# Kernel tuning notes

Hardware: AMD Instinct MI355X
Metric: run time of the kernel (lower is better)

Reference implementation:

```python
import math
import jax, jax.numpy as jnp
import numpy as np

B, QL, CL, D, H = 4, 2048, 2048, 512, 8  # batch, q_len, c_len, hidden/query/context dim, heads
A = D // H
SCALE = 1.0 / math.sqrt(D)
FILL = -100000.0


def setup_inputs() -> dict:
    key = jax.random.key(0)
    ks = jax.random.split(key, 6)
    query = jax.random.normal(ks[0], (B, QL, D), dtype=jnp.float32)
    context = jax.random.normal(ks[1], (B, CL, D), dtype=jnp.float32)
    mask = jax.random.randint(ks[2], (B, CL, H), 0, 2).astype(bool)
    Wq = (jax.random.normal(ks[3], (D, D)) * 0.02).astype(jnp.float32)    # Q: query_dim -> hidden_dim (no bias)
    Wkv = (jax.random.normal(ks[4], (D, 2 * D)) * 0.02).astype(jnp.float32)  # KV: context_dim -> 2*hidden_dim
    Wout = (jax.random.normal(ks[5], (D, D)) * 0.02).astype(jnp.float32)  # out: hidden_dim -> context_dim
    return {"query": query, "context": context, "mask": mask, "Wq": Wq, "Wkv": Wkv, "Wout": Wout}


def reference(query, context, mask, Wq, Wkv, Wout):
    b, q_len, _ = query.shape
    c_len = context.shape[1]
    q = (query @ Wq).reshape(b, q_len, H, A)
    kv = context @ Wkv
    k = kv[..., :D].reshape(b, c_len, H, A)
    v = kv[..., D:].reshape(b, c_len, H, A)
    # [b, q, k, h] scores
    scores = jnp.einsum('bqha,bkha->bqkh', q, k)
    # mask.unsqueeze(1): [b, 1, c_len, h]; apply_mask == where(mask, FILL, x)
    scores = jnp.where(mask[:, None, :, :], FILL, scores)
    attn_weights = jax.nn.softmax(scores * SCALE, axis=2)
    # NOTE: faithful to original torch einsum 'bqkh,bvha->bqha' (k and v are
    # independent summed indices, as in the source code).
    attn = jnp.einsum('bqkh,bvha->bqha', attn_weights, v)
    attn = attn.reshape(b, q_len, D)
    return attn @ Wout
```

## Files before the change

### kernel.cpp

```cpp
#include <hip/hip_runtime.h>

#define BATCH 4
#define QLEN 2048
#define CLEN 2048
#define DIM 512
#define NBLK1 512
#define CPB 128
#define RPC 16
#define NSL 8


__global__ __launch_bounds__(256) void k1_partial(const float* __restrict__ ctx,
                                                  float4* __restrict__ partial) {
    __shared__ float4 red[256];
    const int blk = blockIdx.x, t = threadIdx.x;
    const int b = blk >> 7, ch = blk & 127;
    const int rg = t >> 7, f4 = t & 127;
    const float4* src = reinterpret_cast<const float4*>(ctx)
                      + (size_t)(b * CLEN + ch * RPC) * (DIM / 4);
    float4 s = make_float4(0.f, 0.f, 0.f, 0.f);
#pragma unroll
    for (int i = 0; i < 8; ++i) {
        float4 x = src[(size_t)(rg + 2 * i) * (DIM / 4) + f4];
        s.x += x.x; s.y += x.y; s.z += x.z; s.w += x.w;
    }
    red[t] = s;
    __syncthreads();
    if (t < 128) {
        float4 a = red[t], c = red[t + 128];
        partial[(size_t)blk * (DIM / 4) + t] =
            make_float4(a.x + c.x, a.y + c.y, a.z + c.z, a.w + c.w);
    }
}

__global__ __launch_bounds__(256) void k2_middle(const float4* __restrict__ partial,
                                                 const float* __restrict__ Wkv,
                                                 const float* __restrict__ Wout,
                                                 float* __restrict__ opart) {
    __shared__ float4 red[256];
    __shared__ float cs[DIM];
    __shared__ float vl[256];
    __shared__ float vslice[64];
    const int blk = blockIdx.x, t = threadIdx.x;
    const int b1 = blk >> 3, sl = blk & 7;

    {
        const int g = t & 127, h = t >> 7;
        const float4* p = partial + (size_t)(b1 * CPB + h * 64) * (DIM / 4) + g;
        float4 s = make_float4(0.f, 0.f, 0.f, 0.f);
#pragma unroll 16
        for (int j = 0; j < 64; ++j) {
            float4 x = p[(size_t)j * (DIM / 4)];
            s.x += x.x; s.y += x.y; s.z += x.z; s.w += x.w;
        }
        red[t] = s;
    }
    __syncthreads();
    if (t < 128) {
        float4 a = red[t], c = red[t + 128];
        reinterpret_cast<float4*>(cs)[t] =
            make_float4(a.x + c.x, a.y + c.y, a.z + c.z, a.w + c.w);
    }
    __syncthreads();

    {
        const int el = t & 63, dg = t >> 6;
        const float* w = Wkv + (size_t)(dg * 128) * (2 * DIM) + DIM + sl * 64 + el;
        float s = 0.f;
#pragma unroll 8
        for (int d0 = 0; d0 < 128; ++d0)
            s += cs[dg * 128 + d0] * w[(size_t)d0 * (2 * DIM)];
        vl[t] = s;
    }
    __syncthreads();
    if (t < 64) vslice[t] = vl[t] + vl[t + 64] + vl[t + 128] + vl[t + 192];
    __syncthreads();

    {
#pragma unroll
        for (int half = 0; half < 2; ++half) {
            const int f = half * 256 + t;
            const float* w = Wout + (size_t)(sl * 64) * DIM + f;
            float s = 0.f;
#pragma unroll 8
            for (int e0 = 0; e0 < 64; ++e0)
                s += vslice[e0] * w[(size_t)e0 * DIM];
            opart[(size_t)(sl * BATCH + b1) * DIM + f] = s;
        }
    }
}

__global__ __launch_bounds__(256) void k3_bcast(const float4* __restrict__ opart4,
                                                float4* __restrict__ out) {
    const int blk = blockIdx.x, t = threadIdx.x;
    const int b = blk >> 8, qg = blk & 255;
    const int rg = t >> 7, f4 = t & 127;
    float4 v = make_float4(0.f, 0.f, 0.f, 0.f);
#pragma unroll
    for (int sl = 0; sl < NSL; ++sl) {
        float4 x = opart4[(size_t)(sl * BATCH + b) * (DIM / 4) + f4];
        v.x += x.x; v.y += x.y; v.z += x.z; v.w += x.w;
    }
    float4* dst = out + (size_t)(b * QLEN + qg * 8) * (DIM / 4);
#pragma unroll
    for (int i = 0; i < 4; ++i)
        dst[(size_t)(rg + 2 * i) * (DIM / 4) + f4] = v;
}

extern "C" void kernel_launch(void* const* d_in, const int* in_sizes, int n_in,
                              void* d_out, int out_size, void* d_ws, size_t ws_size,
                              hipStream_t stream) {
    const float* ctx  = (const float*)d_in[1];
    const float* Wkv  = (const float*)d_in[4];
    const float* Wout = (const float*)d_in[5];
    float* ws = (float*)d_ws;
    float* partial = ws;
    float* opart   = partial + (size_t)NBLK1 * DIM;

    k1_partial<<<NBLK1, 256, 0, stream>>>(ctx, (float4*)partial);
    k2_middle<<<BATCH * NSL, 256, 0, stream>>>((const float4*)partial, Wkv, Wout, opart);
    k3_bcast<<<BATCH * 256, 256, 0, stream>>>((const float4*)opart, (float4*)d_out);
}
```

Measured before the change: 26.75 us.

## Precompute Wv·Wout in parallel with context column sums; fuse finish into broadcast

The value half of Wkv is now premultiplied with Wout into a combined 512x512 matrix. That product runs in extra blocks of the same launch as the context column-sum stripes, so it overlaps with the memory-bound reduction. The middle and broadcast kernels merge into one 1024-block kernel: each block recomputes a 32-column slice of the output vector from the summed context and the combined weight, then writes its rows directly. This removes one launch and the serial 32-block middle stage. In exchange it does a full 512x512x512 weight GEMM on every call and repeats the small GEMV work in every finishing block.

New measurement: 35.04 us. +31.0%, slower.

```diff
diff --git a/kernel.cpp b/kernel.cpp
--- a/kernel.cpp
+++ b/kernel.cpp
@@ -4,107 +4,118 @@
 #define QLEN 2048
 #define CLEN 2048
 #define DIM 512
-#define NBLK1 512
-#define CPB 128
-#define RPC 16
-#define NSL 8
+#define NSTRIPE 512
+#define NGEMM 256
+#define NRC 8
 
 
-__global__ __launch_bounds__(256) void k1_partial(const float* __restrict__ ctx,
-                                                  float4* __restrict__ partial) {
-    __shared__ float4 red[256];
+__global__ __launch_bounds__(256) void k1_stripe_gemm(
+    const float* __restrict__ ctx, const float* __restrict__ Wkv,
+    const float* __restrict__ Wout, float4* __restrict__ partial4,
+    float* __restrict__ Wcomb)
+{
     const int blk = blockIdx.x, t = threadIdx.x;
-    const int b = blk >> 7, ch = blk & 127;
-    const int rg = t >> 7, f4 = t & 127;
-    const float4* src = reinterpret_cast<const float4*>(ctx)
-                      + (size_t)(b * CLEN + ch * RPC) * (DIM / 4);
-    float4 s = make_float4(0.f, 0.f, 0.f, 0.f);
+    if (blk < NSTRIPE) {
+        __shared__ float4 red[256];
+        const int b = blk >> 7, rc = (blk >> 4) & 7, cc = blk & 15;
+        const int r0 = t >> 3, c = t & 7;
+        const size_t rowbase = (size_t)(b * CLEN + rc * 256 + r0) * (DIM / 4);
+        const int f4 = cc * 8 + c;
+        float4 s = make_float4(0.f, 0.f, 0.f, 0.f);
 #pragma unroll
-    for (int i = 0; i < 8; ++i) {
-        float4 x = src[(size_t)(rg + 2 * i) * (DIM / 4) + f4];
-        s.x += x.x; s.y += x.y; s.z += x.z; s.w += x.w;
-    }
-    red[t] = s;
-    __syncthreads();
-    if (t < 128) {
-        float4 a = red[t], c = red[t + 128];
-        partial[(size_t)blk * (DIM / 4) + t] =
-            make_float4(a.x + c.x, a.y + c.y, a.z + c.z, a.w + c.w);
+        for (int i = 0; i < 8; ++i) {
+            float4 x = reinterpret_cast<const float4*>(ctx)
+                           [rowbase + (size_t)(32 * i) * (DIM / 4) + f4];
+            s.x += x.x; s.y += x.y; s.z += x.z; s.w += x.w;
+        }
+        red[t] = s;
+        __syncthreads();
+#pragma unroll
+        for (int st = 128; st >= 8; st >>= 1) {
+            if (t < st) {
+                float4 a = red[t], c4 = red[t + st];
+                red[t] = make_float4(a.x + c4.x, a.y + c4.y, a.z + c4.z, a.w + c4.w);
+            }
+            __syncthreads();
+        }
+        if (t < 8)
+            partial4[(size_t)(b * NRC + rc) * (DIM / 4) + cc * 8 + t] = red[t];
+    } else {
+        __shared__ float As[32 * 64];
+        __shared__ float Bs[64 * 32];
+        const int m = blk - NSTRIPE;
+        const int ti = m >> 4, tj = m & 15;
+        const int j = t & 31, i0 = (t >> 5) * 4;
+        float a0 = 0.f, a1 = 0.f, a2 = 0.f, a3 = 0.f;
+        for (int e0 = 0; e0 < DIM; e0 += 64) {
+#pragma unroll
+            for (int it = 0; it < 8; ++it) {
+                const int idx = it * 256 + t;
+                As[idx] = Wkv[(size_t)(ti * 32 + (idx >> 6)) * (2 * DIM) + DIM + e0 + (idx & 63)];
+                Bs[idx] = Wout[(size_t)(e0 + (idx >> 5)) * DIM + tj * 32 + (idx & 31)];
+            }
+            __syncthreads();
+#pragma unroll 16
+            for (int e = 0; e < 64; ++e) {
+                const float bv = Bs[e * 32 + j];
+                a0 += As[(i0 + 0) * 64 + e] * bv;
+                a1 += As[(i0 + 1) * 64 + e] * bv;
+                a2 += As[(i0 + 2) * 64 + e] * bv;
+                a3 += As[(i0 + 3) * 64 + e] * bv;
+            }
+            __syncthreads();
+        }
+        float* dst = Wcomb + (size_t)(ti * 32 + i0) * DIM + tj * 32 + j;
+        dst[0 * DIM] = a0; dst[1 * DIM] = a1; dst[2 * DIM] = a2; dst[3 * DIM] = a3;
     }
 }
 
-__global__ __launch_bounds__(256) void k2_middle(const float4* __restrict__ partial,
-                                                 const float* __restrict__ Wkv,
-                                                 const float* __restrict__ Wout,
-                                                 float* __restrict__ opart) {
-    __shared__ float4 red[256];
+__global__ __launch_bounds__(256) void k2_finish(
+    const float* __restrict__ partial, const float* __restrict__ Wcomb,
+    float4* __restrict__ out)
+{
     __shared__ float cs[DIM];
-    __shared__ float vl[256];
-    __shared__ float vslice[64];
+    __shared__ float rr[256];
+    __shared__ float os[32];
     const int blk = blockIdx.x, t = threadIdx.x;
-    const int b1 = blk >> 3, sl = blk & 7;
+    const int b = blk >> 8, fs = (blk >> 4) & 15, qc = blk & 15;
 
     {
-        const int g = t & 127, h = t >> 7;
-        const float4* p = partial + (size_t)(b1 * CPB + h * 64) * (DIM / 4) + g;
-        float4 s = make_float4(0.f, 0.f, 0.f, 0.f);
-#pragma unroll 16
-        for (int j = 0; j < 64; ++j) {
-            float4 x = p[(size_t)j * (DIM / 4)];
-            s.x += x.x; s.y += x.y; s.z += x.z; s.w += x.w;
+        float s0 = 0.f, s1 = 0.f;
+#pragma unroll
+        for (int rc = 0; rc < NRC; ++rc) {
+            const float* p = partial + (size_t)(b * NRC + rc) * DIM;
+            s0 += p[t]; s1 += p[t + 256];
         }
-        red[t] = s;
-    }
-    __syncthreads();
-    if (t < 128) {
-        float4 a = red[t], c = red[t + 128];
-        reinterpret_cast<float4*>(cs)[t] =
-            make_float4(a.x + c.x, a.y + c.y, a.z + c.z, a.w + c.w);
+        cs[t] = s0; cs[t + 256] = s1;
     }
     __syncthreads();
 
     {
-        const int el = t & 63, dg = t >> 6;
-        const float* w = Wkv + (size_t)(dg * 128) * (2 * DIM) + DIM + sl * 64 + el;
+        const int j = t & 31, dg = t >> 5;
+        const float* w = Wcomb + (size_t)(dg * 64) * DIM + fs * 32 + j;
         float s = 0.f;
 #pragma unroll 8
-        for (int d0 = 0; d0 < 128; ++d0)
-            s += cs[dg * 128 + d0] * w[(size_t)d0 * (2 * DIM)];
-        vl[t] = s;
+        for (int k = 0; k < 64; ++k) s += cs[dg * 64 + k] * w[(size_t)k * DIM];
+        rr[t] = s;
     }
     __syncthreads();
-    if (t < 64) vslice[t] = vl[t] + vl[t + 64] + vl[t + 128] + vl[t + 192];
+    if (t < 32) {
+        float a = 0.f;
+#pragma unroll
+        for (int g = 0; g < 8; ++g) a += rr[g * 32 + t];
+        os[t] = a;
+    }
     __syncthreads();
 
     {
+        const int c = t & 7, q0 = t >> 3;
+        const float4 v = reinterpret_cast<const float4*>(os)[c];
+        float4* dst = out + (size_t)(b * QLEN + qc * 128 + q0) * (DIM / 4) + fs * 8 + c;
 #pragma unroll
-        for (int half = 0; half < 2; ++half) {
-            const int f = half * 256 + t;
-            const float* w = Wout + (size_t)(sl * 64) * DIM + f;
-            float s = 0.f;
-#pragma unroll 8
-            for (int e0 = 0; e0 < 64; ++e0)
-                s += vslice[e0] * w[(size_t)e0 * DIM];
-            opart[(size_t)(sl * BATCH + b1) * DIM + f] = s;
-        }
+        for (int i = 0; i < 4; ++i)
+            dst[(size_t)(32 * i) * (DIM / 4)] = v;
     }
-}
-
-__global__ __launch_bounds__(256) void k3_bcast(const float4* __restrict__ opart4,
-                                                float4* __restrict__ out) {
-    const int blk = blockIdx.x, t = threadIdx.x;
-    const int b = blk >> 8, qg = blk & 255;
-    const int rg = t >> 7, f4 = t & 127;
-    float4 v = make_float4(0.f, 0.f, 0.f, 0.f);
-#pragma unroll
-    for (int sl = 0; sl < NSL; ++sl) {
-        float4 x = opart4[(size_t)(sl * BATCH + b) * (DIM / 4) + f4];
-        v.x += x.x; v.y += x.y; v.z += x.z; v.w += x.w;
-    }
-    float4* dst = out + (size_t)(b * QLEN + qg * 8) * (DIM / 4);
-#pragma unroll
-    for (int i = 0; i < 4; ++i)
-        dst[(size_t)(rg + 2 * i) * (DIM / 4) + f4] = v;
 }
 
 extern "C" void kernel_launch(void* const* d_in, const int* in_sizes, int n_in,
@@ -115,9 +126,9 @@
     const float* Wout = (const float*)d_in[5];
     float* ws = (float*)d_ws;
     float* partial = ws;
-    float* opart   = partial + (size_t)NBLK1 * DIM;
+    float* Wcomb   = partial + BATCH * NRC * DIM;
 
-    k1_partial<<<NBLK1, 256, 0, stream>>>(ctx, (float4*)partial);
-    k2_middle<<<BATCH * NSL, 256, 0, stream>>>((const float4*)partial, Wkv, Wout, opart);
-    k3_bcast<<<BATCH * 256, 256, 0, stream>>>((const float4*)opart, (float4*)d_out);
+    k1_stripe_gemm<<<NSTRIPE + NGEMM, 256, 0, stream>>>(ctx, Wkv, Wout,
+                                                        (float4*)partial, Wcomb);
+    k2_finish<<<1024, 256, 0, stream>>>(partial, Wcomb, (float4*)d_out);
 }
```
